# Kernel optimization log

Hardware: AMD Instinct MI355X
Metric: run time of the kernel (lower is better)

Reference implementation:

```python
import jax, jax.numpy as jnp
import numpy as np

B, P, D, C = 1024, 4, 512, 128  # batch, parts, feat_dim, num_classes


def setup_inputs() -> dict:
    key = jax.random.key(0)
    k1, k2 = jax.random.split(key)
    # scale 0.05 keeps dot products O(1) so exp() stays in fp32 range
    inputs = jax.random.normal(k1, (B, P, D), dtype=jnp.float32) * 0.05
    targets = jax.random.randint(k2, (B,), 0, C, dtype=jnp.int64)
    return {"inputs": inputs, "targets": targets}


def _npairs_loss(inputs, targets):
    b, p, d = inputs.shape
    n = b * p
    X = inputs.reshape(n, d)
    t = jnp.repeat(targets, p)              # (n,) class label per row
    parts = jnp.tile(jnp.arange(p), b)      # (n,) part id per row
    prod = X @ X.T                          # (n, n) similarities

    sc = t[:, None] == t[None, :]           # same class
    sp = parts[:, None] == parts[None, :]   # same attention part
    s_sadc = (~sc) & sp
    s_dasc = sc & (~sp)
    s_dadc = (~sc) & (~sp)

    e_pos = jnp.exp(prod)                   # exp(neg) terms
    e_neg = jnp.exp(-prod)                  # exp(-pos) terms

    def group_loss(pos_mask, neg_mask):
        # sum_i sum_{j in pos_i} log(1 + sum_{k in neg_i} exp(prod[i,k] - prod[i,j]))
        # = sum log1p(S_i * exp(-prod[i,j])) with S_i = sum_{k in neg_i} exp(prod[i,k])
        S = jnp.sum(jnp.where(neg_mask, e_pos, 0.0), axis=1)        # (n,)
        terms = jnp.where(pos_mask, jnp.log1p(S[:, None] * e_neg), 0.0)
        return jnp.sum(terms)

    loss_sadc = group_loss(s_sadc, s_dadc)
    loss_dasc = group_loss(s_dasc, s_dadc)
    # NOTE: original returns loss_sadc twice and never uses loss_sasc (bug kept for fidelity)
    return (loss_sadc + loss_sadc + loss_dasc) / n


def reference(inputs, targets):
    return _npairs_loss(inputs, targets)
```

## Files before the change

kernel.cpp:

```cpp
#include <hip/hip_runtime.h>
#include <stdint.h>

#define GLOBAL_AS __attribute__((address_space(1)))
#define LDS_AS    __attribute__((address_space(3)))

typedef __attribute__((ext_vector_type(8))) __bf16 bf16x8;
typedef __attribute__((ext_vector_type(4))) float  f32x4;

static_assert(sizeof(bf16x8) == 16, "bf16x8 must be 16B");

constexpr int N  = 4096;
constexpr int DK = 512;
constexpr int NTILE = 1056;
constexpr int GRID_MAIN = 1024;
constexpr int PW = 96;


__global__ void k_convert(const float* __restrict__ X, __bf16* __restrict__ Xb,
                          const int* __restrict__ tbuf, int* __restrict__ cls,
                          int* __restrict__ ctr) {
    if (blockIdx.x == 1024) {
        __shared__ int is64;
        const int t = threadIdx.x;
        if (t == 0) { is64 = 1; ctr[0] = GRID_MAIN; }
        __syncthreads();
        if (tbuf[4 * t + 1] != 0 || tbuf[4 * t + 3] != 0) is64 = 0;
        __syncthreads();
        const int f = is64;
#pragma unroll
        for (int q = 0; q < 4; ++q) {
            const int ti = 4 * t + q;
            const int v = tbuf[f ? 2 * ti : ti];
            cls[4 * ti + 0] = v; cls[4 * ti + 1] = v;
            cls[4 * ti + 2] = v; cls[4 * ti + 3] = v;
        }
        return;
    }
    int idx = blockIdx.x * blockDim.x + threadIdx.x;
    const float4* s = (const float4*)X;
    float4 a = s[2 * idx + 0];
    float4 b = s[2 * idx + 1];
    bf16x8 o;
    o[0] = (__bf16)a.x; o[1] = (__bf16)a.y; o[2] = (__bf16)a.z; o[3] = (__bf16)a.w;
    o[4] = (__bf16)b.x; o[5] = (__bf16)b.y; o[6] = (__bf16)b.z; o[7] = (__bf16)b.w;
    *(bf16x8*)(Xb + 8 * idx) = o;
}

__launch_bounds__(256, 4)
__global__ void k_main(const __bf16* __restrict__ Xb, const int* __restrict__ cls,
                       float* __restrict__ partials, int* __restrict__ ctr) {
    __shared__ __align__(16) char smem[3][12288];
    __shared__ int rowcls[128], colcls[64];
    __shared__ int shsteal;
    float4* accR = (float4*)&smem[0][0];
    float4* accC = (float4*)&smem[1][0];

    const int tid  = threadIdx.x;
    const int lane = tid & 63;
    const int wid  = tid >> 6;
    const int wr   = wid >> 1;
    const int wc   = wid & 1;
    const int rA   = lane & 15;
    const int kgrp = lane >> 4;
    const char* xb = (const char*)Xb;

    int tile = (blockIdx.x & 7) * 132 + (blockIdx.x >> 3);

    for (;;) {
        int rt = (int)((sqrtf(4.0f * (float)tile + 1.0f) - 1.0f) * 0.5f);
        while ((rt + 1) * (rt + 2) <= tile) ++rt;
        while (rt * (rt + 1) > tile) --rt;
        const int gc = tile - rt * (rt + 1);
        const int i0 = rt * 128;
        const int j0 = gc * 64;
        const bool fullyBelow = (gc < 2 * rt);

        if (tid < 128) rowcls[tid] = cls[i0 + tid];
        else if (tid < 192) colcls[tid - 128] = cls[j0 + (tid - 128)];
        __syncthreads();

        f32x4 acc[4][2] = {};

#define STAGE(bslot, kt)                                                                   \
        {                                                                                  \
            char* dst = &smem[(bslot)][0];                                                 \
            const size_t kb = (size_t)(kt) * 64;                                           \
            _Pragma("unroll")                                                              \
            for (int q = 0; q < 3; ++q) {                                                  \
                const int l    = q * 256 + tid;                                            \
                const int prow = l >> 2;                                                   \
                const int csrc = (l & 3) ^ ((prow >> 1) & 3);                              \
                const int grow = (prow < 128) ? (i0 + prow) : (j0 + prow - 128);           \
                __builtin_amdgcn_global_load_lds(                                          \
                    (const GLOBAL_AS void*)(xb + (size_t)grow * 1024 + kb + csrc * 16),    \
                    (LDS_AS void*)(dst + q * 4096 + wid * 1024), 16, 0, 0);                \
            }                                                                              \
        }

        STAGE(0, 0);
        STAGE(1, 1);

#pragma unroll
        for (int t = 0; t < 16; ++t) {
            if (t < 15) { asm volatile("s_waitcnt vmcnt(3)" ::: "memory"); }
            else        { asm volatile("s_waitcnt vmcnt(0)" ::: "memory"); }
            __builtin_amdgcn_s_barrier();
            asm volatile("" ::: "memory");
            if (t + 2 < 16) STAGE((t + 2) % 3, t + 2);
            const char* bp = &smem[t % 3][0];
            bf16x8 af[4], bg[2];
#pragma unroll
            for (int m = 0; m < 4; ++m) {
                const int pr = wr * 64 + m * 16 + rA;
                af[m] = *(const bf16x8*)(bp + pr * 64 + ((kgrp ^ ((pr >> 1) & 3)) << 4));
            }
#pragma unroll
            for (int n = 0; n < 2; ++n) {
                const int pr = 128 + wc * 32 + n * 16 + rA;
                bg[n] = *(const bf16x8*)(bp + pr * 64 + ((kgrp ^ ((pr >> 1) & 3)) << 4));
            }
#pragma unroll
            for (int m = 0; m < 4; ++m)
#pragma unroll
                for (int n = 0; n < 2; ++n)
                    acc[m][n] = __builtin_amdgcn_mfma_f32_16x16x32_bf16(bg[n], af[m],
                                                                        acc[m][n], 0, 0, 0);
        }
#undef STAGE

        __syncthreads();

        const int pi = rA & 3;
        int ci[4];
#pragma unroll
        for (int m = 0; m < 4; ++m) ci[m] = rowcls[wr * 64 + m * 16 + rA];
        float rS[4] = {0.f, 0.f, 0.f, 0.f};
        float rP[4] = {0.f, 0.f, 0.f, 0.f};
        float rE[4] = {0.f, 0.f, 0.f, 0.f};
        float rW[4] = {0.f, 0.f, 0.f, 0.f};

#pragma unroll
        for (int n = 0; n < 2; ++n) {
#pragma unroll
            for (int r = 0; r < 4; ++r) {
                const int cj = colcls[wc * 32 + n * 16 + kgrp * 4 + r];
                float cS = 0.f, cP = 0.f, cE = 0.f, cW = 0.f;
#pragma unroll
                for (int m = 0; m < 4; ++m) {
                    const float p  = acc[m][n][r];
                    const float ep = __expf(p);
                    const bool sc = (ci[m] == cj);
                    const bool sp = (pi == r);
                    if (!sc && !sp) { rS[m] += ep; cS += ep; }
                    const float w = (!sc && sp) ? 2.f : ((sc && !sp) ? 1.f : 0.f);
                    rP[m] += w * p;  rE[m] += w * ep;  rW[m] += w;
                    cP += w * p;     cE += w * ep;     cW += w;
                }
                if (fullyBelow) {
#pragma unroll
                    for (int off = 1; off < 16; off <<= 1) {
                        cS += __shfl_xor(cS, off);
                        cP += __shfl_xor(cP, off);
                        cE += __shfl_xor(cE, off);
                        cW += __shfl_xor(cW, off);
                    }
                    if (rA == 0)
                        accC[wr * 64 + wc * 32 + n * 16 + kgrp * 4 + r] =
                            make_float4(cS, cP, cE, cW);
                }
            }
        }
#pragma unroll
        for (int m = 0; m < 4; ++m) {
            float vS = rS[m], vP = rP[m], vE = rE[m], vW = rW[m];
            vS += __shfl_xor(vS, 16); vS += __shfl_xor(vS, 32);
            vP += __shfl_xor(vP, 16); vP += __shfl_xor(vP, 32);
            vE += __shfl_xor(vE, 16); vE += __shfl_xor(vE, 32);
            vW += __shfl_xor(vW, 16); vW += __shfl_xor(vW, 32);
            if (kgrp == 0) accR[wc * 128 + wr * 64 + m * 16 + rA] = make_float4(vS, vP, vE, vW);
        }

        __syncthreads();
        if (tid < 128) {
            float4 a0 = accR[tid], a1 = accR[128 + tid];
            ((float4*)partials)[(size_t)(i0 + tid) * PW + gc] =
                make_float4(a0.x + a1.x, a0.y + a1.y, a0.z + a1.z, a0.w + a1.w);
        } else if (tid < 192 && fullyBelow) {
            const int c = tid - 128;
            float4 c0 = accC[c], c1 = accC[64 + c];
            ((float4*)partials)[(size_t)(j0 + c) * PW + 64 + rt] =
                make_float4(c0.x + c1.x, c0.y + c1.y, c0.z + c1.z, c0.w + c1.w);
        }

        if (tid == 0) shsteal = atomicAdd(ctr, 1);
        __syncthreads();
        const int t2 = shsteal;
        if (t2 >= NTILE) break;
        tile = (t2 & 7) * 132 + (t2 >> 3);
    }
}

__global__ void k_rowloss(const float* __restrict__ partials, float* __restrict__ blockSums) {
    __shared__ float red[4];
    const int tid = threadIdx.x;
    const int lane = tid & 63;
    const int w = tid >> 6;
    const int row = blockIdx.x * 4 + w;
    const int dEnd   = 2 * (row >> 7) + 2;
    const int mStart = ((row >> 6) + 2) >> 1;

    const float4* p = (const float4*)partials + (size_t)row * PW;
    float S = 0.f, P = 0.f, E = 0.f, W_ = 0.f;
#pragma unroll
    for (int s = lane; s < PW; s += 64) {
        const bool valid = (s < 64) ? (s < dEnd) : ((s - 64) >= mStart);
        if (valid) {
            float4 v = p[s];
            S += v.x; P += v.y; E += v.z; W_ += v.w;
        }
    }
#pragma unroll
    for (int off = 1; off < 64; off <<= 1) {
        S += __shfl_xor(S, off);
        P += __shfl_xor(P, off);
        E += __shfl_xor(E, off);
        W_ += __shfl_xor(W_, off);
    }
    if (lane == 0) red[w] = W_ * logf(S) - P + E / S;
    __syncthreads();
    if (tid == 0) blockSums[blockIdx.x] = red[0] + red[1] + red[2] + red[3];
}

__global__ void k_final2(const float* __restrict__ blockSums, float* __restrict__ out) {
    __shared__ float red[4];
    const int t = threadIdx.x;
    float v = blockSums[t] + blockSums[t + 256] + blockSums[t + 512] + blockSums[t + 768];
#pragma unroll
    for (int off = 1; off < 64; off <<= 1) v += __shfl_xor(v, off);
    if ((t & 63) == 0) red[t >> 6] = v;
    __syncthreads();
    if (t == 0) out[0] = (red[0] + red[1] + red[2] + red[3]) / (float)N;
}

extern "C" void kernel_launch(void* const* d_in, const int* in_sizes, int n_in,
                              void* d_out, int out_size, void* d_ws, size_t ws_size,
                              hipStream_t stream) {
    const float* X = (const float*)d_in[0];
    const int*   T = (const int*)d_in[1];
    float* out = (float*)d_out;

    char* ws = (char*)d_ws;
    __bf16* Xb    = (__bf16*)ws;
    int*    cls   = (int*)(ws + (size_t)4 * 1024 * 1024);
    int*    ctr   = (int*)(ws + (size_t)4 * 1024 * 1024 + 16 * 1024);
    float*  parts = (float*)(ws + (size_t)4 * 1024 * 1024 + 16 * 1024 + 256);
    float*  bsums = (float*)ws;

    hipLaunchKernelGGL(k_convert, dim3(1025), dim3(256), 0, stream, X, Xb, T, cls, ctr);
    hipLaunchKernelGGL(k_main,    dim3(GRID_MAIN), dim3(256), 0, stream, Xb, cls, parts, ctr);
    hipLaunchKernelGGL(k_rowloss, dim3(1024), dim3(256), 0, stream, parts, bsums);
    hipLaunchKernelGGL(k_final2,  dim3(1),    dim3(256), 0, stream, bsums, out);
}
```

Baseline: 54.62 us.

## Use 256x128 tiles with 512-thread blocks, one tile per block, drop work stealing

Each block of the main Gram-matrix kernel now covers a 256x128 lower-triangular tile with 8 waves, up from 128x64 with 4 waves. This lowers the number of tiles from 1056 to 272 and removes the persistent loop, the atomic tile counter and its init. Global load addresses are computed once before the k-loop. The partials buffer and row-loss reduction are resized to 48 slots per row. The aim is more operand reuse per staged byte and less scheduling overhead. The cost is 72KB of LDS per block and a 272-block grid that does not divide evenly over the CUs, which can leave a tail.

New measurement: 88.01 us. 61.1% more time.

```diff
diff --git a/kernel.cpp b/kernel.cpp
--- a/kernel.cpp
+++ b/kernel.cpp
@@ -11,18 +11,16 @@
 
 constexpr int N  = 4096;
 constexpr int DK = 512;
-constexpr int NTILE = 1056;
-constexpr int GRID_MAIN = 1024;
-constexpr int PW = 96;
+constexpr int NTILE = 272;
+constexpr int PW = 48;
 
 
 __global__ void k_convert(const float* __restrict__ X, __bf16* __restrict__ Xb,
-                          const int* __restrict__ tbuf, int* __restrict__ cls,
-                          int* __restrict__ ctr) {
+                          const int* __restrict__ tbuf, int* __restrict__ cls) {
     if (blockIdx.x == 1024) {
         __shared__ int is64;
         const int t = threadIdx.x;
-        if (t == 0) { is64 = 1; ctr[0] = GRID_MAIN; }
+        if (t == 0) is64 = 1;
         __syncthreads();
         if (tbuf[4 * t + 1] != 0 || tbuf[4 * t + 3] != 0) is64 = 0;
         __syncthreads();
@@ -46,12 +44,11 @@
     *(bf16x8*)(Xb + 8 * idx) = o;
 }
 
-__launch_bounds__(256, 4)
+__launch_bounds__(512, 4)
 __global__ void k_main(const __bf16* __restrict__ Xb, const int* __restrict__ cls,
-                       float* __restrict__ partials, int* __restrict__ ctr) {
-    __shared__ __align__(16) char smem[3][12288];
-    __shared__ int rowcls[128], colcls[64];
-    __shared__ int shsteal;
+                       float* __restrict__ partials) {
+    __shared__ __align__(16) char smem[3][24576];
+    __shared__ int rowcls[256], colcls[128];
     float4* accR = (float4*)&smem[0][0];
     float4* accC = (float4*)&smem[1][0];
 
@@ -64,139 +61,136 @@
     const int kgrp = lane >> 4;
     const char* xb = (const char*)Xb;
 
-    int tile = (blockIdx.x & 7) * 132 + (blockIdx.x >> 3);
-
-    for (;;) {
-        int rt = (int)((sqrtf(4.0f * (float)tile + 1.0f) - 1.0f) * 0.5f);
-        while ((rt + 1) * (rt + 2) <= tile) ++rt;
-        while (rt * (rt + 1) > tile) --rt;
-        const int gc = tile - rt * (rt + 1);
-        const int i0 = rt * 128;
-        const int j0 = gc * 64;
-        const bool fullyBelow = (gc < 2 * rt);
-
-        if (tid < 128) rowcls[tid] = cls[i0 + tid];
-        else if (tid < 192) colcls[tid - 128] = cls[j0 + (tid - 128)];
-        __syncthreads();
-
-        f32x4 acc[4][2] = {};
-
-#define STAGE(bslot, kt)                                                                   \
-        {                                                                                  \
-            char* dst = &smem[(bslot)][0];                                                 \
-            const size_t kb = (size_t)(kt) * 64;                                           \
-            _Pragma("unroll")                                                              \
-            for (int q = 0; q < 3; ++q) {                                                  \
-                const int l    = q * 256 + tid;                                            \
-                const int prow = l >> 2;                                                   \
-                const int csrc = (l & 3) ^ ((prow >> 1) & 3);                              \
-                const int grow = (prow < 128) ? (i0 + prow) : (j0 + prow - 128);           \
-                __builtin_amdgcn_global_load_lds(                                          \
-                    (const GLOBAL_AS void*)(xb + (size_t)grow * 1024 + kb + csrc * 16),    \
-                    (LDS_AS void*)(dst + q * 4096 + wid * 1024), 16, 0, 0);                \
-            }                                                                              \
-        }
-
-        STAGE(0, 0);
-        STAGE(1, 1);
-
-#pragma unroll
-        for (int t = 0; t < 16; ++t) {
-            if (t < 15) { asm volatile("s_waitcnt vmcnt(3)" ::: "memory"); }
-            else        { asm volatile("s_waitcnt vmcnt(0)" ::: "memory"); }
-            __builtin_amdgcn_s_barrier();
-            asm volatile("" ::: "memory");
-            if (t + 2 < 16) STAGE((t + 2) % 3, t + 2);
-            const char* bp = &smem[t % 3][0];
-            bf16x8 af[4], bg[2];
+    const int bid = (blockIdx.x & 7) * 34 + (blockIdx.x >> 3);
+    int rt = (int)((sqrtf(4.0f * (float)bid + 1.0f) - 1.0f) * 0.5f);
+    while ((rt + 1) * (rt + 2) <= bid) ++rt;
+    while (rt * (rt + 1) > bid) --rt;
+    const int gc = bid - rt * (rt + 1);
+    const int i0 = rt * 256;
+    const int j0 = gc * 128;
+    const bool fullyBelow = (gc < 2 * rt);
+
+    if (tid < 256) rowcls[tid] = cls[i0 + tid];
+    else if (tid < 384) colcls[tid - 256] = cls[j0 + (tid - 256)];
+
+    size_t gbase[3];
+#pragma unroll
+    for (int q = 0; q < 3; ++q) {
+        const int l    = q * 512 + tid;
+        const int prow = l >> 2;
+        const int csrc = (l & 3) ^ ((prow >> 1) & 3);
+        const int grow = (prow < 256) ? (i0 + prow) : (j0 + prow - 256);
+        gbase[q] = (size_t)grow * 1024 + (size_t)(csrc * 16);
+    }
+
+#define STAGE(bslot, kt)                                                       \
+    {                                                                          \
+        char* dst = &smem[(bslot)][0];                                         \
+        const size_t kb = (size_t)(kt) * 64;                                   \
+        _Pragma("unroll")                                                      \
+        for (int q = 0; q < 3; ++q) {                                          \
+            __builtin_amdgcn_global_load_lds(                                  \
+                (const GLOBAL_AS void*)(xb + gbase[q] + kb),                   \
+                (LDS_AS void*)(dst + q * 8192 + wid * 1024), 16, 0, 0);        \
+        }                                                                      \
+    }
+
+    STAGE(0, 0);
+    STAGE(1, 1);
+
+    f32x4 acc[4][4] = {};
+
+#pragma unroll
+    for (int t = 0; t < 16; ++t) {
+        if (t < 15) { asm volatile("s_waitcnt vmcnt(3)" ::: "memory"); }
+        else        { asm volatile("s_waitcnt vmcnt(0)" ::: "memory"); }
+        __builtin_amdgcn_s_barrier();
+        asm volatile("" ::: "memory");
+        if (t + 2 < 16) STAGE((t + 2) % 3, t + 2);
+        const char* bp = &smem[t % 3][0];
+        bf16x8 af[4], bg[4];
+#pragma unroll
+        for (int m = 0; m < 4; ++m) {
+            const int pr = wr * 64 + m * 16 + rA;
+            af[m] = *(const bf16x8*)(bp + pr * 64 + ((kgrp ^ ((pr >> 1) & 3)) << 4));
+        }
+#pragma unroll
+        for (int n = 0; n < 4; ++n) {
+            const int pr = 256 + wc * 64 + n * 16 + rA;
+            bg[n] = *(const bf16x8*)(bp + pr * 64 + ((kgrp ^ ((pr >> 1) & 3)) << 4));
+        }
+#pragma unroll
+        for (int m = 0; m < 4; ++m)
+#pragma unroll
+            for (int n = 0; n < 4; ++n)
+                acc[m][n] = __builtin_amdgcn_mfma_f32_16x16x32_bf16(bg[n], af[m],
+                                                                    acc[m][n], 0, 0, 0);
+    }
+#undef STAGE
+
+    __syncthreads();
+
+    const int pi = rA & 3;
+    int ci[4];
+#pragma unroll
+    for (int m = 0; m < 4; ++m) ci[m] = rowcls[wr * 64 + m * 16 + rA];
+    float rS[4] = {0.f, 0.f, 0.f, 0.f};
+    float rP[4] = {0.f, 0.f, 0.f, 0.f};
+    float rE[4] = {0.f, 0.f, 0.f, 0.f};
+    float rW[4] = {0.f, 0.f, 0.f, 0.f};
+
+#pragma unroll
+    for (int n = 0; n < 4; ++n) {
+#pragma unroll
+        for (int r = 0; r < 4; ++r) {
+            const int cj = colcls[wc * 64 + n * 16 + kgrp * 4 + r];
+            float cS = 0.f, cP = 0.f, cE = 0.f, cW = 0.f;
 #pragma unroll
             for (int m = 0; m < 4; ++m) {
-                const int pr = wr * 64 + m * 16 + rA;
-                af[m] = *(const bf16x8*)(bp + pr * 64 + ((kgrp ^ ((pr >> 1) & 3)) << 4));
+                const float p  = acc[m][n][r];
+                const float ep = __expf(p);
+                const bool sc = (ci[m] == cj);
+                const bool sp = (pi == r);
+                if (!sc && !sp) { rS[m] += ep; cS += ep; }
+                const float w = (!sc && sp) ? 2.f : ((sc && !sp) ? 1.f : 0.f);
+                rP[m] += w * p;  rE[m] += w * ep;  rW[m] += w;
+                cP += w * p;     cE += w * ep;     cW += w;
             }
-#pragma unroll
-            for (int n = 0; n < 2; ++n) {
-                const int pr = 128 + wc * 32 + n * 16 + rA;
-                bg[n] = *(const bf16x8*)(bp + pr * 64 + ((kgrp ^ ((pr >> 1) & 3)) << 4));
+            if (fullyBelow) {
+#pragma unroll
+                for (int off = 1; off < 16; off <<= 1) {
+                    cS += __shfl_xor(cS, off);
+                    cP += __shfl_xor(cP, off);
+                    cE += __shfl_xor(cE, off);
+                    cW += __shfl_xor(cW, off);
+                }
+                if (rA == 0)
+                    accC[wr * 128 + wc * 64 + n * 16 + kgrp * 4 + r] =
+                        make_float4(cS, cP, cE, cW);
             }
-#pragma unroll
-            for (int m = 0; m < 4; ++m)
-#pragma unroll
-                for (int n = 0; n < 2; ++n)
-                    acc[m][n] = __builtin_amdgcn_mfma_f32_16x16x32_bf16(bg[n], af[m],
-                                                                        acc[m][n], 0, 0, 0);
-        }
-#undef STAGE
-
-        __syncthreads();
-
-        const int pi = rA & 3;
-        int ci[4];
-#pragma unroll
-        for (int m = 0; m < 4; ++m) ci[m] = rowcls[wr * 64 + m * 16 + rA];
-        float rS[4] = {0.f, 0.f, 0.f, 0.f};
-        float rP[4] = {0.f, 0.f, 0.f, 0.f};
-        float rE[4] = {0.f, 0.f, 0.f, 0.f};
-        float rW[4] = {0.f, 0.f, 0.f, 0.f};
-
-#pragma unroll
-        for (int n = 0; n < 2; ++n) {
-#pragma unroll
-            for (int r = 0; r < 4; ++r) {
-                const int cj = colcls[wc * 32 + n * 16 + kgrp * 4 + r];
-                float cS = 0.f, cP = 0.f, cE = 0.f, cW = 0.f;
-#pragma unroll
-                for (int m = 0; m < 4; ++m) {
-                    const float p  = acc[m][n][r];
-                    const float ep = __expf(p);
-                    const bool sc = (ci[m] == cj);
-                    const bool sp = (pi == r);
-                    if (!sc && !sp) { rS[m] += ep; cS += ep; }
-                    const float w = (!sc && sp) ? 2.f : ((sc && !sp) ? 1.f : 0.f);
-                    rP[m] += w * p;  rE[m] += w * ep;  rW[m] += w;
-                    cP += w * p;     cE += w * ep;     cW += w;
-                }
-                if (fullyBelow) {
-#pragma unroll
-                    for (int off = 1; off < 16; off <<= 1) {
-                        cS += __shfl_xor(cS, off);
-                        cP += __shfl_xor(cP, off);
-                        cE += __shfl_xor(cE, off);
-                        cW += __shfl_xor(cW, off);
-                    }
-                    if (rA == 0)
-                        accC[wr * 64 + wc * 32 + n * 16 + kgrp * 4 + r] =
-                            make_float4(cS, cP, cE, cW);
-                }
-            }
-        }
-#pragma unroll
-        for (int m = 0; m < 4; ++m) {
-            float vS = rS[m], vP = rP[m], vE = rE[m], vW = rW[m];
-            vS += __shfl_xor(vS, 16); vS += __shfl_xor(vS, 32);
-            vP += __shfl_xor(vP, 16); vP += __shfl_xor(vP, 32);
-            vE += __shfl_xor(vE, 16); vE += __shfl_xor(vE, 32);
-            vW += __shfl_xor(vW, 16); vW += __shfl_xor(vW, 32);
-            if (kgrp == 0) accR[wc * 128 + wr * 64 + m * 16 + rA] = make_float4(vS, vP, vE, vW);
-        }
-
-        __syncthreads();
-        if (tid < 128) {
-            float4 a0 = accR[tid], a1 = accR[128 + tid];
-            ((float4*)partials)[(size_t)(i0 + tid) * PW + gc] =
-                make_float4(a0.x + a1.x, a0.y + a1.y, a0.z + a1.z, a0.w + a1.w);
-        } else if (tid < 192 && fullyBelow) {
-            const int c = tid - 128;
-            float4 c0 = accC[c], c1 = accC[64 + c];
-            ((float4*)partials)[(size_t)(j0 + c) * PW + 64 + rt] =
-                make_float4(c0.x + c1.x, c0.y + c1.y, c0.z + c1.z, c0.w + c1.w);
-        }
-
-        if (tid == 0) shsteal = atomicAdd(ctr, 1);
-        __syncthreads();
-        const int t2 = shsteal;
-        if (t2 >= NTILE) break;
-        tile = (t2 & 7) * 132 + (t2 >> 3);
+        }
+    }
+#pragma unroll
+    for (int m = 0; m < 4; ++m) {
+        float vS = rS[m], vP = rP[m], vE = rE[m], vW = rW[m];
+        vS += __shfl_xor(vS, 16); vS += __shfl_xor(vS, 32);
+        vP += __shfl_xor(vP, 16); vP += __shfl_xor(vP, 32);
+        vE += __shfl_xor(vE, 16); vE += __shfl_xor(vE, 32);
+        vW += __shfl_xor(vW, 16); vW += __shfl_xor(vW, 32);
+        if (kgrp == 0) accR[wc * 256 + wr * 64 + m * 16 + rA] = make_float4(vS, vP, vE, vW);
+    }
+
+    __syncthreads();
+    if (tid < 256) {
+        float4 a0 = accR[tid], a1 = accR[256 + tid];
+        ((float4*)partials)[(size_t)(i0 + tid) * PW + gc] =
+            make_float4(a0.x + a1.x, a0.y + a1.y, a0.z + a1.z, a0.w + a1.w);
+    } else if (tid < 384 && fullyBelow) {
+        const int c = tid - 256;
+        float4 c0 = accC[c], c1 = accC[128 + c], c2 = accC[256 + c], c3 = accC[384 + c];
+        ((float4*)partials)[(size_t)(j0 + c) * PW + 32 + rt] =
+            make_float4(c0.x + c1.x + c2.x + c3.x, c0.y + c1.y + c2.y + c3.y,
+                        c0.z + c1.z + c2.z + c3.z, c0.w + c1.w + c2.w + c3.w);
     }
 }
 
@@ -206,17 +200,16 @@
     const int lane = tid & 63;
     const int w = tid >> 6;
     const int row = blockIdx.x * 4 + w;
-    const int dEnd   = 2 * (row >> 7) + 2;
-    const int mStart = ((row >> 6) + 2) >> 1;
+    const int dEnd   = 2 * (row >> 8) + 2;
+    const int mStart = ((row >> 7) + 2) >> 1;
 
     const float4* p = (const float4*)partials + (size_t)row * PW;
     float S = 0.f, P = 0.f, E = 0.f, W_ = 0.f;
-#pragma unroll
-    for (int s = lane; s < PW; s += 64) {
-        const bool valid = (s < 64) ? (s < dEnd) : ((s - 64) >= mStart);
+    if (lane < PW) {
+        const bool valid = (lane < 32) ? (lane < dEnd) : ((lane - 32) >= mStart);
         if (valid) {
-            float4 v = p[s];
-            S += v.x; P += v.y; E += v.z; W_ += v.w;
+            float4 v = p[lane];
+            S = v.x; P = v.y; E = v.z; W_ = v.w;
         }
     }
 #pragma unroll
@@ -252,12 +245,11 @@
     char* ws = (char*)d_ws;
     __bf16* Xb    = (__bf16*)ws;
     int*    cls   = (int*)(ws + (size_t)4 * 1024 * 1024);
-    int*    ctr   = (int*)(ws + (size_t)4 * 1024 * 1024 + 16 * 1024);
-    float*  parts = (float*)(ws + (size_t)4 * 1024 * 1024 + 16 * 1024 + 256);
+    float*  parts = (float*)(ws + (size_t)4 * 1024 * 1024 + 16 * 1024);
     float*  bsums = (float*)ws;
 
-    hipLaunchKernelGGL(k_convert, dim3(1025), dim3(256), 0, stream, X, Xb, T, cls, ctr);
-    hipLaunchKernelGGL(k_main,    dim3(GRID_MAIN), dim3(256), 0, stream, Xb, cls, parts, ctr);
-    hipLaunchKernelGGL(k_rowloss, dim3(1024), dim3(256), 0, stream, parts, bsums);
-    hipLaunchKernelGGL(k_final2,  dim3(1),    dim3(256), 0, stream, bsums, out);
-}
+    hipLaunchKernelGGL(k_convert, dim3(1025),  dim3(256), 0, stream, X, Xb, T, cls);
+    hipLaunchKernelGGL(k_main,    dim3(NTILE), dim3(512), 0, stream, Xb, cls, parts);
+    hipLaunchKernelGGL(k_rowloss, dim3(1024),  dim3(256), 0, stream, parts, bsums);
+    hipLaunchKernelGGL(k_final2,  dim3(1),     dim3(256), 0, stream, bsums, out);
+}
```

## Enlarge Gram tiles to 128x128 with 512-thread blocks and transposed partials

Applied to the files above, without the earlier changes.

Changes the symmetric X·Xᵀ tiling from 128x64 tiles to square 128x128 lower-triangle tiles, cutting the tile count roughly in half, and processes each with 8 waves per block. Global-to-LDS staging addresses are precomputed once per tile. Partials are now stored slice-major so the row-loss kernel reads them coalesced with one thread per row. The reductions in the last two kernels are simplified to match. The larger blocks use more LDS and registers per block, and fewer tiles make load balancing coarser across CUs.

Measured after the change: 51.99 us. 1.05x faster.

```diff
diff --git a/kernel.cpp b/kernel.cpp
--- a/kernel.cpp
+++ b/kernel.cpp
@@ -11,9 +11,9 @@
 
 constexpr int N  = 4096;
 constexpr int DK = 512;
-constexpr int NTILE = 1056;
-constexpr int GRID_MAIN = 1024;
-constexpr int PW = 96;
+constexpr int NTILE = 528;
+constexpr int GRID_MAIN = 512;
+constexpr int PW = 32;
 
 
 __global__ void k_convert(const float* __restrict__ X, __bf16* __restrict__ Xb,
@@ -46,11 +46,11 @@
     *(bf16x8*)(Xb + 8 * idx) = o;
 }
 
-__launch_bounds__(256, 4)
+__launch_bounds__(512, 4)
 __global__ void k_main(const __bf16* __restrict__ Xb, const int* __restrict__ cls,
                        float* __restrict__ partials, int* __restrict__ ctr) {
-    __shared__ __align__(16) char smem[3][12288];
-    __shared__ int rowcls[128], colcls[64];
+    __shared__ __align__(16) char smem[3][16384];
+    __shared__ int rowcls[128], colcls[128];
     __shared__ int shsteal;
     float4* accR = (float4*)&smem[0][0];
     float4* accC = (float4*)&smem[1][0];
@@ -58,51 +58,57 @@
     const int tid  = threadIdx.x;
     const int lane = tid & 63;
     const int wid  = tid >> 6;
-    const int wr   = wid >> 1;
-    const int wc   = wid & 1;
+    const int wr   = wid >> 2;
+    const int wc   = wid & 3;
     const int rA   = lane & 15;
     const int kgrp = lane >> 4;
     const char* xb = (const char*)Xb;
 
-    int tile = (blockIdx.x & 7) * 132 + (blockIdx.x >> 3);
+    int tile = (blockIdx.x & 7) * 66 + (blockIdx.x >> 3);
 
     for (;;) {
-        int rt = (int)((sqrtf(4.0f * (float)tile + 1.0f) - 1.0f) * 0.5f);
-        while ((rt + 1) * (rt + 2) <= tile) ++rt;
-        while (rt * (rt + 1) > tile) --rt;
-        const int gc = tile - rt * (rt + 1);
+        int rt = (int)((sqrtf(8.0f * (float)tile + 1.0f) - 1.0f) * 0.5f);
+        while (((rt + 1) * (rt + 2)) / 2 <= tile) ++rt;
+        while ((rt * (rt + 1)) / 2 > tile) --rt;
+        const int g  = tile - (rt * (rt + 1)) / 2;
         const int i0 = rt * 128;
-        const int j0 = gc * 64;
-        const bool fullyBelow = (gc < 2 * rt);
-
-        if (tid < 128) rowcls[tid] = cls[i0 + tid];
-        else if (tid < 192) colcls[tid - 128] = cls[j0 + (tid - 128)];
-        __syncthreads();
-
-        f32x4 acc[4][2] = {};
-
-#define STAGE(bslot, kt)                                                                   \
-        {                                                                                  \
-            char* dst = &smem[(bslot)][0];                                                 \
-            const size_t kb = (size_t)(kt) * 64;                                           \
-            _Pragma("unroll")                                                              \
-            for (int q = 0; q < 3; ++q) {                                                  \
-                const int l    = q * 256 + tid;                                            \
-                const int prow = l >> 2;                                                   \
-                const int csrc = (l & 3) ^ ((prow >> 1) & 3);                              \
-                const int grow = (prow < 128) ? (i0 + prow) : (j0 + prow - 128);           \
-                __builtin_amdgcn_global_load_lds(                                          \
-                    (const GLOBAL_AS void*)(xb + (size_t)grow * 1024 + kb + csrc * 16),    \
-                    (LDS_AS void*)(dst + q * 4096 + wid * 1024), 16, 0, 0);                \
-            }                                                                              \
+        const int j0 = g * 128;
+        const bool offdiag = (rt != g);
+
+        if (tid < 128)      rowcls[tid] = cls[i0 + tid];
+        else if (tid < 256) colcls[tid - 128] = cls[j0 + (tid - 128)];
+        __syncthreads();
+
+        size_t gbase[2];
+#pragma unroll
+        for (int q = 0; q < 2; ++q) {
+            const int l    = q * 512 + tid;
+            const int prow = l >> 2;
+            const int csrc = (l & 3) ^ ((prow >> 1) & 3);
+            const int grow = (prow < 128) ? (i0 + prow) : (j0 + prow - 128);
+            gbase[q] = (size_t)grow * 1024 + (size_t)(csrc * 16);
+        }
+
+#define STAGE(bslot, kt)                                                       \
+        {                                                                      \
+            char* dst = &smem[(bslot)][0];                                     \
+            const size_t kb = (size_t)(kt) * 64;                               \
+            _Pragma("unroll")                                                  \
+            for (int q = 0; q < 2; ++q) {                                      \
+                __builtin_amdgcn_global_load_lds(                              \
+                    (const GLOBAL_AS void*)(xb + gbase[q] + kb),               \
+                    (LDS_AS void*)(dst + q * 8192 + tid * 16), 16, 0, 0);      \
+            }                                                                  \
         }
 
         STAGE(0, 0);
         STAGE(1, 1);
 
+        f32x4 acc[4][2] = {};
+
 #pragma unroll
         for (int t = 0; t < 16; ++t) {
-            if (t < 15) { asm volatile("s_waitcnt vmcnt(3)" ::: "memory"); }
+            if (t < 15) { asm volatile("s_waitcnt vmcnt(2)" ::: "memory"); }
             else        { asm volatile("s_waitcnt vmcnt(0)" ::: "memory"); }
             __builtin_amdgcn_s_barrier();
             asm volatile("" ::: "memory");
@@ -156,7 +162,7 @@
                     rP[m] += w * p;  rE[m] += w * ep;  rW[m] += w;
                     cP += w * p;     cE += w * ep;     cW += w;
                 }
-                if (fullyBelow) {
+                if (offdiag) {
 #pragma unroll
                     for (int off = 1; off < 16; off <<= 1) {
                         cS += __shfl_xor(cS, off);
@@ -165,7 +171,7 @@
                         cW += __shfl_xor(cW, off);
                     }
                     if (rA == 0)
-                        accC[wr * 64 + wc * 32 + n * 16 + kgrp * 4 + r] =
+                        accC[wr * 128 + wc * 32 + n * 16 + kgrp * 4 + r] =
                             make_float4(cS, cP, cE, cW);
                 }
             }
@@ -177,18 +183,21 @@
             vP += __shfl_xor(vP, 16); vP += __shfl_xor(vP, 32);
             vE += __shfl_xor(vE, 16); vE += __shfl_xor(vE, 32);
             vW += __shfl_xor(vW, 16); vW += __shfl_xor(vW, 32);
-            if (kgrp == 0) accR[wc * 128 + wr * 64 + m * 16 + rA] = make_float4(vS, vP, vE, vW);
+            if (kgrp == 0)
+                accR[wc * 128 + wr * 64 + m * 16 + rA] = make_float4(vS, vP, vE, vW);
         }
 
         __syncthreads();
         if (tid < 128) {
-            float4 a0 = accR[tid], a1 = accR[128 + tid];
-            ((float4*)partials)[(size_t)(i0 + tid) * PW + gc] =
-                make_float4(a0.x + a1.x, a0.y + a1.y, a0.z + a1.z, a0.w + a1.w);
-        } else if (tid < 192 && fullyBelow) {
+            float4 a0 = accR[tid],       a1 = accR[128 + tid];
+            float4 a2 = accR[256 + tid], a3 = accR[384 + tid];
+            ((float4*)partials)[(size_t)g * N + i0 + tid] =
+                make_float4(a0.x + a1.x + a2.x + a3.x, a0.y + a1.y + a2.y + a3.y,
+                            a0.z + a1.z + a2.z + a3.z, a0.w + a1.w + a2.w + a3.w);
+        } else if (tid < 256 && offdiag) {
             const int c = tid - 128;
-            float4 c0 = accC[c], c1 = accC[64 + c];
-            ((float4*)partials)[(size_t)(j0 + c) * PW + 64 + rt] =
+            float4 c0 = accC[c], c1 = accC[128 + c];
+            ((float4*)partials)[(size_t)rt * N + j0 + c] =
                 make_float4(c0.x + c1.x, c0.y + c1.y, c0.z + c1.z, c0.w + c1.w);
         }
 
@@ -196,50 +205,37 @@
         __syncthreads();
         const int t2 = shsteal;
         if (t2 >= NTILE) break;
-        tile = (t2 & 7) * 132 + (t2 >> 3);
+        const int e = t2 - GRID_MAIN;
+        tile = (e >> 1) * 66 + 64 + (e & 1);
     }
 }
 
 __global__ void k_rowloss(const float* __restrict__ partials, float* __restrict__ blockSums) {
-    __shared__ float red[4];
+    __shared__ float red[256];
     const int tid = threadIdx.x;
-    const int lane = tid & 63;
-    const int w = tid >> 6;
-    const int row = blockIdx.x * 4 + w;
-    const int dEnd   = 2 * (row >> 7) + 2;
-    const int mStart = ((row >> 6) + 2) >> 1;
-
-    const float4* p = (const float4*)partials + (size_t)row * PW;
-    float S = 0.f, P = 0.f, E = 0.f, W_ = 0.f;
-#pragma unroll
-    for (int s = lane; s < PW; s += 64) {
-        const bool valid = (s < 64) ? (s < dEnd) : ((s - 64) >= mStart);
-        if (valid) {
-            float4 v = p[s];
-            S += v.x; P += v.y; E += v.z; W_ += v.w;
-        }
-    }
-#pragma unroll
-    for (int off = 1; off < 64; off <<= 1) {
-        S += __shfl_xor(S, off);
-        P += __shfl_xor(P, off);
-        E += __shfl_xor(E, off);
-        W_ += __shfl_xor(W_, off);
-    }
-    if (lane == 0) red[w] = W_ * logf(S) - P + E / S;
+    const int row = blockIdx.x * 256 + tid;
+    const float4* p = (const float4*)partials;
+    float S = 0.f, P = 0.f, E = 0.f, W = 0.f;
+#pragma unroll
+    for (int s = 0; s < PW; ++s) {
+        float4 v = p[(size_t)s * N + row];
+        S += v.x; P += v.y; E += v.z; W += v.w;
+    }
+    red[tid] = W * logf(S) - P + E / S;
     __syncthreads();
-    if (tid == 0) blockSums[blockIdx.x] = red[0] + red[1] + red[2] + red[3];
+    for (int s = 128; s > 0; s >>= 1) {
+        if (tid < s) red[tid] += red[tid + s];
+        __syncthreads();
+    }
+    if (tid == 0) blockSums[blockIdx.x] = red[0];
 }
 
 __global__ void k_final2(const float* __restrict__ blockSums, float* __restrict__ out) {
-    __shared__ float red[4];
     const int t = threadIdx.x;
-    float v = blockSums[t] + blockSums[t + 256] + blockSums[t + 512] + blockSums[t + 768];
-#pragma unroll
-    for (int off = 1; off < 64; off <<= 1) v += __shfl_xor(v, off);
-    if ((t & 63) == 0) red[t >> 6] = v;
-    __syncthreads();
-    if (t == 0) out[0] = (red[0] + red[1] + red[2] + red[3]) / (float)N;
+    float v = (t < 16) ? blockSums[t] : 0.f;
+#pragma unroll
+    for (int off = 1; off < 16; off <<= 1) v += __shfl_xor(v, off);
+    if (t == 0) out[0] = v / (float)N;
 }
 
 extern "C" void kernel_launch(void* const* d_in, const int* in_sizes, int n_in,
@@ -256,8 +252,8 @@
     float*  parts = (float*)(ws + (size_t)4 * 1024 * 1024 + 16 * 1024 + 256);
     float*  bsums = (float*)ws;
 
-    hipLaunchKernelGGL(k_convert, dim3(1025), dim3(256), 0, stream, X, Xb, T, cls, ctr);
-    hipLaunchKernelGGL(k_main,    dim3(GRID_MAIN), dim3(256), 0, stream, Xb, cls, parts, ctr);
-    hipLaunchKernelGGL(k_rowloss, dim3(1024), dim3(256), 0, stream, parts, bsums);
-    hipLaunchKernelGGL(k_final2,  dim3(1),    dim3(256), 0, stream, bsums, out);
-}
+    hipLaunchKernelGGL(k_convert, dim3(1025),      dim3(256), 0, stream, X, Xb, T, cls, ctr);
+    hipLaunchKernelGGL(k_main,    dim3(GRID_MAIN), dim3(512), 0, stream, Xb, cls, parts, ctr);
+    hipLaunchKernelGGL(k_rowloss, dim3(16),        dim3(256), 0, stream, parts, bsums);
+    hipLaunchKernelGGL(k_final2,  dim3(1),         dim3(64),  0, stream, bsums, out);
+}
```
